# Performance work log

Hardware: AMD Instinct MI355X
Metric: run time of the kernel (lower is better)

## Reference

```python
import jax, jax.numpy as jnp
import numpy as np

# Straight-through sign binarization: forward -> {-1, +1}, backward -> identity
@jax.custom_vjp
def binarize(x):
    return jnp.where(x >= 0, jnp.ones_like(x), -jnp.ones_like(x))

def _bin_fwd(x):
    return binarize(x), None

def _bin_bwd(res, g):
    return (g,)

binarize.defvjp(_bin_fwd, _bin_bwd)

BATCH = 16384
IN_SIZE = 1025   # must be 2**n + 1
HIDDEN = 1025    # must be 2**n + 1

def setup_inputs() -> dict:
    key = jax.random.key(0)
    k0, k1, k2, k3 = jax.random.split(key, 4)
    # weight init scale per reset_parameters: sqrt(1.5/(in+out)) uniform
    s = float(np.sqrt(1.5 / (IN_SIZE + HIDDEN)))
    return {
        "x": jax.random.normal(k0, (BATCH, IN_SIZE), dtype=jnp.float32),
        "W0": jax.random.uniform(k1, (HIDDEN, IN_SIZE), jnp.float32, -s, s),
        "W1": jax.random.uniform(k2, (HIDDEN, HIDDEN), jnp.float32, -s, s),
        "W2": jax.random.uniform(k3, (1, HIDDEN), jnp.float32, -s, s),
    }

def reference(x, W0, W1, W2):
    # x: [B, IN_SIZE]; weights stored [out, in] (nn.Linear convention), no bias
    h = x.reshape(-1, IN_SIZE)
    for W in (W0, W1, W2):
        lin = h @ binarize(W).T          # float GEMM against +/-1 weights
        h = binarize(lin)                # sign activation
    # num_classes == 2 path: to_boolean maps {-1,+1} -> {0,1}, then squeeze
    out = (h + 1.0) * 0.5
    return out.squeeze(-1)               # [B]
```

## Files before the change

### kernel.cpp

```cpp
#include <hip/hip_runtime.h>
#include <cstdint>

typedef unsigned long long u64;
typedef unsigned short ushort_t;
typedef __attribute__((ext_vector_type(8))) short short8;
typedef __attribute__((ext_vector_type(4))) float f32x4;

#define B_TOTAL 16384
#define K_DIM   1025
#define O_DIM   1025
#define NWORDS  17
#define NKT     34
#define NFRAG   72
#define A_BYTES 8192
#define B_BYTES 73728
#define SMEM_BYTES 99328
#define FLAG_CAP 4096
#define L23_ROWS 16

__device__ __forceinline__ ushort_t f2bf_rne(float f) {
  unsigned u = __float_as_uint(f);
  return (ushort_t)((u + 0x7fffu + ((u >> 16) & 1u)) >> 16);
}

__global__ __launch_bounds__(256) void pack_all_kernel(const float* __restrict__ W0,
                                                       const float* __restrict__ W1,
                                                       const float* __restrict__ W2,
                                                       u64* __restrict__ w0b,
                                                       u64* __restrict__ w1b,
                                                       u64* __restrict__ w2b) {
  __shared__ unsigned char by[136];
  const int row = blockIdx.x, t = threadIdx.x;
  const float* src; u64* dst; int o;
  if (row < O_DIM)           { src = W0; dst = w0b; o = row; }
  else if (row < 2 * O_DIM)  { src = W1; dst = w1b; o = row - O_DIM; }
  else                       { src = W2; dst = w2b; o = 0; }
  if (t < 136) {
    const float* wr = src + (size_t)o * K_DIM;
    unsigned m = 0;
#pragma unroll
    for (int j = 0; j < 8; ++j) {
      int k = t * 8 + j;
      bool pos = (k < K_DIM) ? (wr[k] >= 0.0f) : true;
      m |= (unsigned)pos << j;
    }
    by[t] = (unsigned char)m;
  }
  __syncthreads();
  if (t < NWORDS) {
    u64 word = 0;
#pragma unroll
    for (int q = 0; q < 8; ++q) word |= (u64)by[t * 8 + q] << (8 * q);
    dst[(size_t)o * NWORDS + t] = word;
  }
}

__global__ __launch_bounds__(256) void prep_sbf_kernel(const float* __restrict__ w0,
                                                       ushort_t* __restrict__ sbf) {
  const int t = threadIdx.x;
  const int f = blockIdx.x * 4 + (t >> 6);
  const int lane = t & 63;
  const int kt = f / NFRAG, nf = f % NFRAG;
  const int o = nf * 16 + (lane & 15);
  const int kbase = kt * 32 + (lane >> 4) * 8;
  short8 sv;
#pragma unroll
  for (int j = 0; j < 8; ++j) {
    int k = kbase + j;
    short v = 0;
    if (o < O_DIM && k < K_DIM)
      v = (short)((w0[(size_t)o * K_DIM + k] >= 0.0f) ? 0x3F80 : 0xBF80);
    sv[j] = v;
  }
  *(short8*)&sbf[(size_t)f * 512 + lane * 8] = sv;
}

__global__ __launch_bounds__(512, 1) void l1_fused_kernel(
    const ushort_t* __restrict__ sbf, const float* __restrict__ x,
    const u64* __restrict__ w0b, u64* __restrict__ h1b) {
  extern __shared__ char smem[];
  const int p = blockIdx.x;
  const int t = threadIdx.x;
  const int wave = t >> 6, lane = t & 63;
  const int lr = lane & 15, lg = lane >> 4;
  const int b0 = p * 64;
  const int obase = wave * 144;

  const int u = t & 255;
  const int cmf = u >> 6, clane = u & 63;
  const int crow = cmf * 16 + (clane & 15);
  const int ckb0 = (clane >> 4) * 8;
  const bool isLo = (t >= 256);
  const float* xrowC = x + (size_t)(b0 + crow) * K_DIM;
  const int convOff = (isLo ? 4096 : 0) + cmf * 1024 + clane * 16;

  const ushort_t* gB = sbf + (size_t)(wave * 9) * 512 + lane * 8;

  f32x4 acc[4][9];
#pragma unroll
  for (int mf = 0; mf < 4; ++mf)
#pragma unroll
    for (int nfl = 0; nfl < 9; ++nfl)
#pragma unroll
      for (int c = 0; c < 4; ++c) acc[mf][nfl][c] = 0.0f;

  float xv[8];
  float sAcc = 0.0f;
  short8 bX[9];

#define LOADX(KT)                                                              \
  {                                                                            \
    int kb = (KT) * 32 + ckb0;                                                 \
    const float* xr = xrowC + kb;                                              \
    if (kb + 8 <= K_DIM) {                                                     \
      float4 a = *(const float4*)xr;                                           \
      float4 b = *(const float4*)(xr + 4);                                     \
      xv[0]=a.x; xv[1]=a.y; xv[2]=a.z; xv[3]=a.w;                              \
      xv[4]=b.x; xv[5]=b.y; xv[6]=b.z; xv[7]=b.w;                              \
    } else {                                                                   \
      _Pragma("unroll")                                                        \
      for (int j = 0; j < 8; ++j) xv[j] = (kb + j < K_DIM) ? xr[j] : 0.0f;     \
    }                                                                          \
  }

#define CONVERT_WRITE(DBUF)                                                    \
  {                                                                            \
    short8 w8;                                                                 \
    if (!isLo) {                                                               \
      _Pragma("unroll")                                                        \
      for (int j = 0; j < 8; ++j) {                                            \
        float v = xv[j];                                                       \
        sAcc += fabsf(v);                                                      \
        w8[j] = (short)f2bf_rne(v);                                            \
      }                                                                        \
    } else {                                                                   \
      _Pragma("unroll")                                                        \
      for (int j = 0; j < 8; ++j) {                                            \
        float v = xv[j];                                                       \
        ushort_t h = f2bf_rne(v);                                              \
        float hf = __uint_as_float((unsigned)h << 16);                         \
        w8[j] = (short)f2bf_rne(v - hf);                                       \
      }                                                                        \
    }                                                                          \
    *(short8*)((DBUF) + convOff) = w8;                                         \
  }

#define LOADB(KT)                                                              \
  {                                                                            \
    _Pragma("unroll")                                                          \
    for (int i = 0; i < 9; ++i)                                                \
      bX[i] = *(const short8*)&gB[(size_t)(KT) * (B_BYTES / 2) + i * 512];     \
  }

#define MFMA_STEP(AOFF)                                                        \
  {                                                                            \
    const ushort_t* A = (const ushort_t*)(smem + (AOFF));                      \
    short8 ah[4], al[4];                                                       \
    _Pragma("unroll")                                                          \
    for (int mf = 0; mf < 4; ++mf) {                                           \
      ah[mf] = *(const short8*)&A[mf * 512 + lane * 8];                        \
      al[mf] = *(const short8*)&A[(4 + mf) * 512 + lane * 8];                  \
    }                                                                          \
    _Pragma("unroll")                                                          \
    for (int nfl = 0; nfl < 9; ++nfl) {                                        \
      _Pragma("unroll")                                                        \
      for (int mf = 0; mf < 4; ++mf) {                                         \
        acc[mf][nfl] = __builtin_amdgcn_mfma_f32_16x16x32_bf16(ah[mf], bX[nfl], acc[mf][nfl], 0, 0, 0); \
        acc[mf][nfl] = __builtin_amdgcn_mfma_f32_16x16x32_bf16(al[mf], bX[nfl], acc[mf][nfl], 0, 0, 0); \
      }                                                                        \
    }                                                                          \
  }

  LOADX(0); CONVERT_WRITE(smem);
  LOADB(0);
  __syncthreads();

  for (int kt = 0; kt < NKT; kt += 2) {
    {
      LOADX(kt + 1);
      MFMA_STEP(0);
      LOADB(kt + 1);
      CONVERT_WRITE(smem + 8192);
      __syncthreads();
    }
    {
      if (kt + 2 < NKT) LOADX(kt + 2);
      MFMA_STEP(8192);
      if (kt + 2 < NKT) { LOADB(kt + 2); CONVERT_WRITE(smem + 0); }
      __syncthreads();
    }
  }
#undef LOADX
#undef CONVERT_WRITE
#undef LOADB
#undef MFMA_STEP

  unsigned char* bits = (unsigned char*)smem;
  u64*      hs    = (u64*)(smem + 73728);
  unsigned* list  = (unsigned*)(smem + 82432);
  unsigned* lcnt  = (unsigned*)(smem + 98816);
  float*    errbL = (float*)(smem + 98832);
  unsigned* hsw   = (unsigned*)hs;

  sAcc += __shfl_xor(sAcc, 16, 64);
  sAcc += __shfl_xor(sAcc, 32, 64);
  if (t == 0) *lcnt = 0;
  if (!isLo && lg == 0)
    errbL[crow] = sAcc * (1.02f / 65536.0f) + 0.125f;
  __syncthreads();

  float eb[4][4];
#pragma unroll
  for (int mf = 0; mf < 4; ++mf)
#pragma unroll
    for (int rg = 0; rg < 4; ++rg) eb[mf][rg] = errbL[mf * 16 + lg * 4 + rg];

#pragma unroll
  for (int mf = 0; mf < 4; ++mf)
#pragma unroll
    for (int nfl = 0; nfl < 9; ++nfl)
#pragma unroll
      for (int rg = 0; rg < 4; ++rg) {
        int bl = mf * 16 + lg * 4 + rg;
        int o  = obase + nfl * 16 + lr;
        float lin = acc[mf][nfl][rg];
        unsigned abit = (lin >= 0.0f) ? 1u : 0u;
        bits[bl * 1152 + o] = (unsigned char)abit;
        if ((o < O_DIM) && (fabsf(lin) <= eb[mf][rg])) {
          unsigned idx = atomicAdd(lcnt, 1u);
          if (idx < FLAG_CAP)
            list[idx] = ((unsigned)bl << 12) | ((unsigned)o << 1) | abit;
        }
      }
  __syncthreads();

  for (int task = t; task < 64 * NWORDS; task += 512) {
    int row = task / NWORDS, w = task % NWORDS;
    u64 word = 0;
#pragma unroll
    for (int q = 0; q < 8; ++q) {
      u64 v = *(const u64*)&bits[row * 1152 + w * 64 + q * 8];
#pragma unroll
      for (int m = 0; m < 8; ++m)
        word |= ((v >> (8 * m)) & 1ull) << (q * 8 + m);
    }
    int rem = O_DIM - w * 64;
    if (rem < 64) word |= (~0ull << rem);
    hs[row * NWORDS + w] = word;
  }
  __syncthreads();

  {
    unsigned n = *lcnt; if (n > FLAG_CAP) n = FLAG_CAP;
    for (unsigned i = t; i < n; i += 512) {
      unsigned en = list[i];
      int bl = (int)(en >> 12), o = (int)((en >> 1) & 0x7ffu);
      unsigned abit = en & 1u;
      const float* xr = x + (size_t)(b0 + bl) * K_DIM;
      const u64* wr = w0b + (size_t)o * NWORDS;
      float a = 0.0f;
      for (int j = 0; j < 16; ++j) {
        u64 wd = wr[j];
#pragma unroll
        for (int m = 0; m < 64; ++m) {
          float v = xr[j * 64 + m];
          unsigned neg = ((unsigned)(wd >> m) & 1u) ^ 1u;
          a += __uint_as_float(__float_as_uint(v) ^ (neg << 31));
        }
      }
      {
        u64 wd = wr[16];
        float v = xr[1024];
        unsigned neg = ((unsigned)wd & 1u) ^ 1u;
        a += __uint_as_float(__float_as_uint(v) ^ (neg << 31));
      }
      unsigned nb = (a >= 0.0f) ? 1u : 0u;
      if (nb != abit)
        atomicXor(&hsw[bl * 34 + (o >> 5)], 1u << (o & 31));
    }
  }
  __syncthreads();

  for (int task = t; task < 64 * NWORDS; task += 512)
    h1b[(size_t)b0 * NWORDS + task] = hs[task];
}

__global__ __launch_bounds__(256) void l2l3_kernel(const u64* __restrict__ h1b,
                                                   const u64* __restrict__ w1b,
                                                   const u64* __restrict__ w2b,
                                                   float* __restrict__ out) {
  __shared__ u64 hs[L23_ROWS][NWORDS];
  __shared__ u64 h2[L23_ROWS][NWORDS];
  const int bt = blockIdx.x;
  const int t = threadIdx.x;
  for (int i = t; i < L23_ROWS * NWORDS; i += 256)
    hs[i / NWORDS][i % NWORDS] = h1b[(size_t)(bt * L23_ROWS + i / NWORDS) * NWORDS + i % NWORDS];
  __syncthreads();

  const int w = t >> 6, l = t & 63;
  for (int oc = w; oc < NWORDS; oc += 4) {
    int o = oc * 64 + l;
    bool valid = (o < O_DIM);
    int orow = valid ? o : (O_DIM - 1);
    u64 wb[NWORDS];
#pragma unroll
    for (int j = 0; j < NWORDS; ++j) wb[j] = w1b[(size_t)orow * NWORDS + j];
    for (int b = 0; b < L23_ROWS; b += 2) {
      int p0 = 0, p1 = 0;
#pragma unroll
      for (int j = 0; j < NWORDS; ++j) {
        p0 += __popcll(hs[b + 0][j] ^ wb[j]);
        p1 += __popcll(hs[b + 1][j] ^ wb[j]);
      }
      u64 m0 = __ballot(valid ? (K_DIM - 2 * p0 >= 0) : true);
      u64 m1 = __ballot(valid ? (K_DIM - 2 * p1 >= 0) : true);
      if (l == 0) h2[b + 0][oc] = m0;
      if (l == 1) h2[b + 1][oc] = m1;
    }
  }
  __syncthreads();
  if (t < L23_ROWS) {
    int p = 0;
#pragma unroll
    for (int j = 0; j < NWORDS; ++j) p += __popcll(h2[t][j] ^ w2b[j]);
    out[bt * L23_ROWS + t] = ((K_DIM - 2 * p) >= 0) ? 1.0f : 0.0f;
  }
}

extern "C" void kernel_launch(void* const* d_in, const int* in_sizes, int n_in,
                              void* d_out, int out_size, void* d_ws, size_t ws_size,
                              hipStream_t stream) {
  const float* x  = (const float*)d_in[0];
  const float* W0 = (const float*)d_in[1];
  const float* W1 = (const float*)d_in[2];
  const float* W2 = (const float*)d_in[3];
  float* out = (float*)d_out;

  char* ws = (char*)d_ws;
  u64*      w0b  = (u64*)(ws);
  u64*      w1b  = (u64*)(ws + 139776);
  u64*      w2b  = (u64*)(ws + 279552);
  u64*      h1b  = (u64*)(ws + 280064);
  ushort_t* sbf  = (ushort_t*)(ws + 2508288);

  static bool attr_set = false;
  if (!attr_set) {
    hipFuncSetAttribute((const void*)l1_fused_kernel,
                        hipFuncAttributeMaxDynamicSharedMemorySize, SMEM_BYTES);
    attr_set = true;
  }

  pack_all_kernel<<<2 * O_DIM + 1, 256, 0, stream>>>(W0, W1, W2, w0b, w1b, w2b);
  prep_sbf_kernel<<<NKT * NFRAG / 4, 256, 0, stream>>>(W0, sbf);
  l1_fused_kernel<<<B_TOTAL / 64, 512, SMEM_BYTES, stream>>>(sbf, x, w0b, h1b);
  l2l3_kernel<<<B_TOTAL / L23_ROWS, 256, 0, stream>>>(h1b, w1b, w2b, out);
}
```

Baseline: 153.3 us.

## Split layer-1 GEMM output columns across three blocks to raise occupancy

The fused layer-1 kernel now launches a 2D grid where each block computes one third of the output columns (384) for its 64 batch rows, cutting accumulators from 36 to 12 fragments per wave and shared memory from ~97KB to ~36KB. Launch bounds change to allow 4 blocks per CU, so more waves can hide memory latency. The cost is that each x tile is loaded and bf16-split three times (once per column slice), the error-bound reduction is recomputed per block, and the bit-packing, flag list and fix-up are adjusted to per-slice indexing with a smaller flag capacity.

```diff
diff --git a/kernel.cpp b/kernel.cpp
--- a/kernel.cpp
+++ b/kernel.cpp
@@ -14,8 +14,9 @@
 #define NFRAG   72
 #define A_BYTES 8192
 #define B_BYTES 73728
-#define SMEM_BYTES 99328
-#define FLAG_CAP 4096
+#define NS      3
+#define SMEM_BYTES 36352
+#define FLAG_CAP 2048
 #define L23_ROWS 16
 
 __device__ __forceinline__ ushort_t f2bf_rne(float f) {
@@ -75,16 +76,16 @@
   *(short8*)&sbf[(size_t)f * 512 + lane * 8] = sv;
 }
 
-__global__ __launch_bounds__(512, 1) void l1_fused_kernel(
+__global__ __launch_bounds__(512, 4) void l1_fused_kernel(
     const ushort_t* __restrict__ sbf, const float* __restrict__ x,
     const u64* __restrict__ w0b, u64* __restrict__ h1b) {
   extern __shared__ char smem[];
-  const int p = blockIdx.x;
+  const int p = blockIdx.x, ns = blockIdx.y;
   const int t = threadIdx.x;
   const int wave = t >> 6, lane = t & 63;
   const int lr = lane & 15, lg = lane >> 4;
   const int b0 = p * 64;
-  const int obase = wave * 144;
+  const int obase_l = wave * 48;
 
   const int u = t & 255;
   const int cmf = u >> 6, clane = u & 63;
@@ -94,19 +95,19 @@
   const float* xrowC = x + (size_t)(b0 + crow) * K_DIM;
   const int convOff = (isLo ? 4096 : 0) + cmf * 1024 + clane * 16;
 
-  const ushort_t* gB = sbf + (size_t)(wave * 9) * 512 + lane * 8;
-
-  f32x4 acc[4][9];
+  const ushort_t* gB = sbf + (size_t)(ns * 24 + wave * 3) * 512 + lane * 8;
+
+  f32x4 acc[4][3];
 #pragma unroll
   for (int mf = 0; mf < 4; ++mf)
 #pragma unroll
-    for (int nfl = 0; nfl < 9; ++nfl)
+    for (int nfl = 0; nfl < 3; ++nfl)
 #pragma unroll
       for (int c = 0; c < 4; ++c) acc[mf][nfl][c] = 0.0f;
 
   float xv[8];
   float sAcc = 0.0f;
-  short8 bX[9];
+  short8 bX[3];
 
 #define LOADX(KT)                                                              \
   {                                                                            \
@@ -148,25 +149,29 @@
 #define LOADB(KT)                                                              \
   {                                                                            \
     _Pragma("unroll")                                                          \
-    for (int i = 0; i < 9; ++i)                                                \
+    for (int i = 0; i < 3; ++i)                                                \
       bX[i] = *(const short8*)&gB[(size_t)(KT) * (B_BYTES / 2) + i * 512];     \
   }
 
 #define MFMA_STEP(AOFF)                                                        \
   {                                                                            \
     const ushort_t* A = (const ushort_t*)(smem + (AOFF));                      \
-    short8 ah[4], al[4];                                                       \
     _Pragma("unroll")                                                          \
-    for (int mf = 0; mf < 4; ++mf) {                                           \
-      ah[mf] = *(const short8*)&A[mf * 512 + lane * 8];                        \
-      al[mf] = *(const short8*)&A[(4 + mf) * 512 + lane * 8];                  \
-    }                                                                          \
-    _Pragma("unroll")                                                          \
-    for (int nfl = 0; nfl < 9; ++nfl) {                                        \
-      _Pragma("unroll")                                                        \
-      for (int mf = 0; mf < 4; ++mf) {                                         \
-        acc[mf][nfl] = __builtin_amdgcn_mfma_f32_16x16x32_bf16(ah[mf], bX[nfl], acc[mf][nfl], 0, 0, 0); \
-        acc[mf][nfl] = __builtin_amdgcn_mfma_f32_16x16x32_bf16(al[mf], bX[nfl], acc[mf][nfl], 0, 0, 0); \
+    for (int h = 0; h < 2; ++h) {                                              \
+      short8 ah2[2], al2[2];                                                   \
+      _Pragma("unroll")                                                        \
+      for (int m2 = 0; m2 < 2; ++m2) {                                         \
+        ah2[m2] = *(const short8*)&A[(h * 2 + m2) * 512 + lane * 8];           \
+        al2[m2] = *(const short8*)&A[(4 + h * 2 + m2) * 512 + lane * 8];       \
+      }                                                                        \
+      _Pragma("unroll")                                                        \
+      for (int nfl = 0; nfl < 3; ++nfl) {                                      \
+        _Pragma("unroll")                                                      \
+        for (int m2 = 0; m2 < 2; ++m2) {                                       \
+          int mf = h * 2 + m2;                                                 \
+          acc[mf][nfl] = __builtin_amdgcn_mfma_f32_16x16x32_bf16(ah2[m2], bX[nfl], acc[mf][nfl], 0, 0, 0); \
+          acc[mf][nfl] = __builtin_amdgcn_mfma_f32_16x16x32_bf16(al2[m2], bX[nfl], acc[mf][nfl], 0, 0, 0); \
+        }                                                                      \
       }                                                                        \
     }                                                                          \
   }
@@ -196,10 +201,10 @@
 #undef MFMA_STEP
 
   unsigned char* bits = (unsigned char*)smem;
-  u64*      hs    = (u64*)(smem + 73728);
-  unsigned* list  = (unsigned*)(smem + 82432);
-  unsigned* lcnt  = (unsigned*)(smem + 98816);
-  float*    errbL = (float*)(smem + 98832);
+  u64*      hs    = (u64*)(smem + 24576);
+  unsigned* list  = (unsigned*)(smem + 27648);
+  unsigned* lcnt  = (unsigned*)(smem + 35840);
+  float*    errbL = (float*)(smem + 35844);
   unsigned* hsw   = (unsigned*)hs;
 
   sAcc += __shfl_xor(sAcc, 16, 64);
@@ -218,35 +223,38 @@
 #pragma unroll
   for (int mf = 0; mf < 4; ++mf)
 #pragma unroll
-    for (int nfl = 0; nfl < 9; ++nfl)
+    for (int nfl = 0; nfl < 3; ++nfl)
 #pragma unroll
       for (int rg = 0; rg < 4; ++rg) {
         int bl = mf * 16 + lg * 4 + rg;
-        int o  = obase + nfl * 16 + lr;
+        int ol = obase_l + nfl * 16 + lr;
+        int og = ns * 384 + ol;
         float lin = acc[mf][nfl][rg];
         unsigned abit = (lin >= 0.0f) ? 1u : 0u;
-        bits[bl * 1152 + o] = (unsigned char)abit;
-        if ((o < O_DIM) && (fabsf(lin) <= eb[mf][rg])) {
+        bits[bl * 384 + ol] = (unsigned char)abit;
+        if ((og < O_DIM) && (fabsf(lin) <= eb[mf][rg])) {
           unsigned idx = atomicAdd(lcnt, 1u);
           if (idx < FLAG_CAP)
-            list[idx] = ((unsigned)bl << 12) | ((unsigned)o << 1) | abit;
+            list[idx] = ((unsigned)bl << 12) | ((unsigned)ol << 1) | abit;
         }
       }
   __syncthreads();
 
-  for (int task = t; task < 64 * NWORDS; task += 512) {
-    int row = task / NWORDS, w = task % NWORDS;
+  if (t < 64 * 6) {
+    int row = t / 6, w = t % 6;
+    int widx = ns * 6 + w;
     u64 word = 0;
 #pragma unroll
     for (int q = 0; q < 8; ++q) {
-      u64 v = *(const u64*)&bits[row * 1152 + w * 64 + q * 8];
+      u64 v = *(const u64*)&bits[row * 384 + w * 64 + q * 8];
 #pragma unroll
       for (int m = 0; m < 8; ++m)
         word |= ((v >> (8 * m)) & 1ull) << (q * 8 + m);
     }
-    int rem = O_DIM - w * 64;
-    if (rem < 64) word |= (~0ull << rem);
-    hs[row * NWORDS + w] = word;
+    int rem = O_DIM - widx * 64;
+    if (rem <= 0) word = ~0ull;
+    else if (rem < 64) word |= (~0ull << rem);
+    hs[row * 6 + w] = word;
   }
   __syncthreads();
 
@@ -254,10 +262,11 @@
     unsigned n = *lcnt; if (n > FLAG_CAP) n = FLAG_CAP;
     for (unsigned i = t; i < n; i += 512) {
       unsigned en = list[i];
-      int bl = (int)(en >> 12), o = (int)((en >> 1) & 0x7ffu);
+      int bl = (int)(en >> 12), ol = (int)((en >> 1) & 0x7ffu);
+      int og = ns * 384 + ol;
       unsigned abit = en & 1u;
       const float* xr = x + (size_t)(b0 + bl) * K_DIM;
-      const u64* wr = w0b + (size_t)o * NWORDS;
+      const u64* wr = w0b + (size_t)og * NWORDS;
       float a = 0.0f;
       for (int j = 0; j < 16; ++j) {
         u64 wd = wr[j];
@@ -276,13 +285,17 @@
       }
       unsigned nb = (a >= 0.0f) ? 1u : 0u;
       if (nb != abit)
-        atomicXor(&hsw[bl * 34 + (o >> 5)], 1u << (o & 31));
-    }
-  }
-  __syncthreads();
-
-  for (int task = t; task < 64 * NWORDS; task += 512)
-    h1b[(size_t)b0 * NWORDS + task] = hs[task];
+        atomicXor(&hsw[bl * 12 + (ol >> 5)], 1u << (ol & 31));
+    }
+  }
+  __syncthreads();
+
+  if (t < 64 * 6) {
+    int row = t / 6, w = t % 6;
+    int widx = ns * 6 + w;
+    if (widx < NWORDS)
+      h1b[(size_t)(b0 + row) * NWORDS + widx] = hs[t];
+  }
 }
 
 __global__ __launch_bounds__(256) void l2l3_kernel(const u64* __restrict__ h1b,
@@ -352,6 +365,6 @@
 
   pack_all_kernel<<<2 * O_DIM + 1, 256, 0, stream>>>(W0, W1, W2, w0b, w1b, w2b);
   prep_sbf_kernel<<<NKT * NFRAG / 4, 256, 0, stream>>>(W0, sbf);
-  l1_fused_kernel<<<B_TOTAL / 64, 512, SMEM_BYTES, stream>>>(sbf, x, w0b, h1b);
+  l1_fused_kernel<<<dim3(B_TOTAL / 64, NS), 512, SMEM_BYTES, stream>>>(sbf, x, w0b, h1b);
   l2l3_kernel<<<B_TOTAL / L23_ROWS, 256, 0, stream>>>(h1b, w1b, w2b, out);
 }
```

Result: slower. 217.9 us (+42.1%).

## Halve layer-1 row tile to 32 and stream B fragments to raise occupancy

Applied to the files above, without the earlier changes.

Shrinks the fused layer-1 GEMM tile from 64 to 32 batch rows per block, halving accumulators and LDS (about 49KB instead of 99KB). The launch bound moves from 1 to 4 blocks per CU and the grid doubles. B fragments are no longer held in a full 9-register prefetch; they are loaded from global memory through a 4-deep rotating register window inside the MFMA step. The intent is more resident waves to hide latency, at the cost of each B fragment being read from global/L2 twice as often across the grid.

```diff
diff --git a/kernel.cpp b/kernel.cpp
--- a/kernel.cpp
+++ b/kernel.cpp
@@ -4,6 +4,7 @@
 typedef unsigned long long u64;
 typedef unsigned short ushort_t;
 typedef __attribute__((ext_vector_type(8))) short short8;
+typedef __attribute__((ext_vector_type(4))) short short4v;
 typedef __attribute__((ext_vector_type(4))) float f32x4;
 
 #define B_TOTAL 16384
@@ -12,10 +13,10 @@
 #define NWORDS  17
 #define NKT     34
 #define NFRAG   72
-#define A_BYTES 8192
 #define B_BYTES 73728
-#define SMEM_BYTES 99328
-#define FLAG_CAP 4096
+#define BM      32
+#define SMEM_BYTES 49920
+#define FLAG_CAP 2048
 #define L23_ROWS 16
 
 __device__ __forceinline__ ushort_t f2bf_rne(float f) {
@@ -75,7 +76,7 @@
   *(short8*)&sbf[(size_t)f * 512 + lane * 8] = sv;
 }
 
-__global__ __launch_bounds__(512, 1) void l1_fused_kernel(
+__global__ __launch_bounds__(512, 4) void l1_fused_kernel(
     const ushort_t* __restrict__ sbf, const float* __restrict__ x,
     const u64* __restrict__ w0b, u64* __restrict__ h1b) {
   extern __shared__ char smem[];
@@ -83,140 +84,134 @@
   const int t = threadIdx.x;
   const int wave = t >> 6, lane = t & 63;
   const int lr = lane & 15, lg = lane >> 4;
-  const int b0 = p * 64;
+  const int b0 = p * BM;
   const int obase = wave * 144;
 
   const int u = t & 255;
-  const int cmf = u >> 6, clane = u & 63;
+  const int slot = u >> 1, half = u & 1;
+  const int cmf = slot >> 6, clane = slot & 63;
   const int crow = cmf * 16 + (clane & 15);
-  const int ckb0 = (clane >> 4) * 8;
+  const int ckb0 = (clane >> 4) * 8 + half * 4;
   const bool isLo = (t >= 256);
   const float* xrowC = x + (size_t)(b0 + crow) * K_DIM;
-  const int convOff = (isLo ? 4096 : 0) + cmf * 1024 + clane * 16;
+  const int convOff = (isLo ? 2048 : 0) + cmf * 1024 + clane * 16 + half * 8;
 
   const ushort_t* gB = sbf + (size_t)(wave * 9) * 512 + lane * 8;
 
-  f32x4 acc[4][9];
-#pragma unroll
-  for (int mf = 0; mf < 4; ++mf)
+  f32x4 acc[2][9];
+#pragma unroll
+  for (int mf = 0; mf < 2; ++mf)
 #pragma unroll
     for (int nfl = 0; nfl < 9; ++nfl)
 #pragma unroll
       for (int c = 0; c < 4; ++c) acc[mf][nfl][c] = 0.0f;
 
-  float xv[8];
+  float xv[4];
   float sAcc = 0.0f;
-  short8 bX[9];
 
 #define LOADX(KT)                                                              \
   {                                                                            \
     int kb = (KT) * 32 + ckb0;                                                 \
     const float* xr = xrowC + kb;                                              \
-    if (kb + 8 <= K_DIM) {                                                     \
+    if (kb + 4 <= K_DIM) {                                                     \
       float4 a = *(const float4*)xr;                                           \
-      float4 b = *(const float4*)(xr + 4);                                     \
-      xv[0]=a.x; xv[1]=a.y; xv[2]=a.z; xv[3]=a.w;                              \
-      xv[4]=b.x; xv[5]=b.y; xv[6]=b.z; xv[7]=b.w;                              \
+      xv[0] = a.x; xv[1] = a.y; xv[2] = a.z; xv[3] = a.w;                      \
     } else {                                                                   \
       _Pragma("unroll")                                                        \
-      for (int j = 0; j < 8; ++j) xv[j] = (kb + j < K_DIM) ? xr[j] : 0.0f;     \
+      for (int j = 0; j < 4; ++j) xv[j] = (kb + j < K_DIM) ? xr[j] : 0.0f;     \
     }                                                                          \
   }
 
 #define CONVERT_WRITE(DBUF)                                                    \
   {                                                                            \
-    short8 w8;                                                                 \
+    short4v w4;                                                                \
     if (!isLo) {                                                               \
       _Pragma("unroll")                                                        \
-      for (int j = 0; j < 8; ++j) {                                            \
+      for (int j = 0; j < 4; ++j) {                                            \
         float v = xv[j];                                                       \
         sAcc += fabsf(v);                                                      \
-        w8[j] = (short)f2bf_rne(v);                                            \
+        w4[j] = (short)f2bf_rne(v);                                            \
       }                                                                        \
     } else {                                                                   \
       _Pragma("unroll")                                                        \
-      for (int j = 0; j < 8; ++j) {                                            \
+      for (int j = 0; j < 4; ++j) {                                            \
         float v = xv[j];                                                       \
         ushort_t h = f2bf_rne(v);                                              \
         float hf = __uint_as_float((unsigned)h << 16);                         \
-        w8[j] = (short)f2bf_rne(v - hf);                                       \
+        w4[j] = (short)f2bf_rne(v - hf);                                       \
       }                                                                        \
     }                                                                          \
-    *(short8*)((DBUF) + convOff) = w8;                                         \
-  }
-
-#define LOADB(KT)                                                              \
-  {                                                                            \
-    _Pragma("unroll")                                                          \
-    for (int i = 0; i < 9; ++i)                                                \
-      bX[i] = *(const short8*)&gB[(size_t)(KT) * (B_BYTES / 2) + i * 512];     \
-  }
-
-#define MFMA_STEP(AOFF)                                                        \
+    *(short4v*)((DBUF) + convOff) = w4;                                        \
+  }
+
+#define MFMA_STEP(AOFF, KT)                                                    \
   {                                                                            \
     const ushort_t* A = (const ushort_t*)(smem + (AOFF));                      \
-    short8 ah[4], al[4];                                                       \
-    _Pragma("unroll")                                                          \
-    for (int mf = 0; mf < 4; ++mf) {                                           \
-      ah[mf] = *(const short8*)&A[mf * 512 + lane * 8];                        \
-      al[mf] = *(const short8*)&A[(4 + mf) * 512 + lane * 8];                  \
-    }                                                                          \
+    const ushort_t* gBkt = gB + (size_t)(KT) * (B_BYTES / 2);                  \
+    short8 ah0 = *(const short8*)&A[lane * 8];                                 \
+    short8 ah1 = *(const short8*)&A[512 + lane * 8];                           \
+    short8 al0 = *(const short8*)&A[1024 + lane * 8];                          \
+    short8 al1 = *(const short8*)&A[1536 + lane * 8];                          \
+    short8 bR[4];                                                              \
+    bR[0] = *(const short8*)&gBkt[0];                                          \
+    bR[1] = *(const short8*)&gBkt[512];                                        \
+    bR[2] = *(const short8*)&gBkt[1024];                                       \
     _Pragma("unroll")                                                          \
     for (int nfl = 0; nfl < 9; ++nfl) {                                        \
-      _Pragma("unroll")                                                        \
-      for (int mf = 0; mf < 4; ++mf) {                                         \
-        acc[mf][nfl] = __builtin_amdgcn_mfma_f32_16x16x32_bf16(ah[mf], bX[nfl], acc[mf][nfl], 0, 0, 0); \
-        acc[mf][nfl] = __builtin_amdgcn_mfma_f32_16x16x32_bf16(al[mf], bX[nfl], acc[mf][nfl], 0, 0, 0); \
-      }                                                                        \
+      if (nfl < 6) bR[(nfl + 3) & 3] = *(const short8*)&gBkt[(nfl + 3) * 512]; \
+      short8 bv = bR[nfl & 3];                                                 \
+      acc[0][nfl] = __builtin_amdgcn_mfma_f32_16x16x32_bf16(ah0, bv, acc[0][nfl], 0, 0, 0); \
+      acc[0][nfl] = __builtin_amdgcn_mfma_f32_16x16x32_bf16(al0, bv, acc[0][nfl], 0, 0, 0); \
+      acc[1][nfl] = __builtin_amdgcn_mfma_f32_16x16x32_bf16(ah1, bv, acc[1][nfl], 0, 0, 0); \
+      acc[1][nfl] = __builtin_amdgcn_mfma_f32_16x16x32_bf16(al1, bv, acc[1][nfl], 0, 0, 0); \
     }                                                                          \
   }
 
   LOADX(0); CONVERT_WRITE(smem);
-  LOADB(0);
   __syncthreads();
 
   for (int kt = 0; kt < NKT; kt += 2) {
-    {
-      LOADX(kt + 1);
-      MFMA_STEP(0);
-      LOADB(kt + 1);
-      CONVERT_WRITE(smem + 8192);
-      __syncthreads();
-    }
-    {
-      if (kt + 2 < NKT) LOADX(kt + 2);
-      MFMA_STEP(8192);
-      if (kt + 2 < NKT) { LOADB(kt + 2); CONVERT_WRITE(smem + 0); }
-      __syncthreads();
-    }
+    LOADX(kt + 1);
+    MFMA_STEP(0, kt);
+    CONVERT_WRITE(smem + 4096);
+    __syncthreads();
+    if (kt + 2 < NKT) LOADX(kt + 2);
+    MFMA_STEP(4096, kt + 1);
+    if (kt + 2 < NKT) CONVERT_WRITE(smem);
+    __syncthreads();
   }
 #undef LOADX
 #undef CONVERT_WRITE
-#undef LOADB
 #undef MFMA_STEP
 
   unsigned char* bits = (unsigned char*)smem;
-  u64*      hs    = (u64*)(smem + 73728);
-  unsigned* list  = (unsigned*)(smem + 82432);
-  unsigned* lcnt  = (unsigned*)(smem + 98816);
-  float*    errbL = (float*)(smem + 98832);
+  u64*      hs    = (u64*)(smem + 36864);
+  unsigned* list  = (unsigned*)(smem + 41216);
+  unsigned* lcnt  = (unsigned*)(smem + 49408);
+  float*    errbP = (float*)(smem + 49412);
+  float*    errbL = (float*)(smem + 49668);
   unsigned* hsw   = (unsigned*)hs;
 
-  sAcc += __shfl_xor(sAcc, 16, 64);
+  sAcc += __shfl_xor(sAcc, 1, 64);
   sAcc += __shfl_xor(sAcc, 32, 64);
   if (t == 0) *lcnt = 0;
-  if (!isLo && lg == 0)
-    errbL[crow] = sAcc * (1.02f / 65536.0f) + 0.125f;
-  __syncthreads();
-
-  float eb[4][4];
-#pragma unroll
-  for (int mf = 0; mf < 4; ++mf)
+  if (!isLo && (lane & 1) == 0 && lane < 32)
+    errbP[wave * 16 + (lane >> 1)] = sAcc;
+  __syncthreads();
+  if (t < BM) {
+    int cm = t >> 4, R = t & 15;
+    errbL[t] = (errbP[cm * 32 + R] + errbP[cm * 32 + 16 + R]) * (1.02f / 65536.0f) + 0.125f;
+  }
+  __syncthreads();
+
+  float eb[2][4];
+#pragma unroll
+  for (int mf = 0; mf < 2; ++mf)
 #pragma unroll
     for (int rg = 0; rg < 4; ++rg) eb[mf][rg] = errbL[mf * 16 + lg * 4 + rg];
 
 #pragma unroll
-  for (int mf = 0; mf < 4; ++mf)
+  for (int mf = 0; mf < 2; ++mf)
 #pragma unroll
     for (int nfl = 0; nfl < 9; ++nfl)
 #pragma unroll
@@ -234,7 +229,7 @@
       }
   __syncthreads();
 
-  for (int task = t; task < 64 * NWORDS; task += 512) {
+  for (int task = t; task < BM * NWORDS; task += 512) {
     int row = task / NWORDS, w = task % NWORDS;
     u64 word = 0;
 #pragma unroll
@@ -246,7 +241,7 @@
     }
     int rem = O_DIM - w * 64;
     if (rem < 64) word |= (~0ull << rem);
-    hs[row * NWORDS + w] = word;
+    hs[task] = word;
   }
   __syncthreads();
 
@@ -281,7 +276,7 @@
   }
   __syncthreads();
 
-  for (int task = t; task < 64 * NWORDS; task += 512)
+  for (int task = t; task < BM * NWORDS; task += 512)
     h1b[(size_t)b0 * NWORDS + task] = hs[task];
 }
 
@@ -352,6 +347,6 @@
 
   pack_all_kernel<<<2 * O_DIM + 1, 256, 0, stream>>>(W0, W1, W2, w0b, w1b, w2b);
   prep_sbf_kernel<<<NKT * NFRAG / 4, 256, 0, stream>>>(W0, sbf);
-  l1_fused_kernel<<<B_TOTAL / 64, 512, SMEM_BYTES, stream>>>(sbf, x, w0b, h1b);
+  l1_fused_kernel<<<B_TOTAL / BM, 512, SMEM_BYTES, stream>>>(sbf, x, w0b, h1b);
   l2l3_kernel<<<B_TOTAL / L23_ROWS, 256, 0, stream>>>(h1b, w1b, w2b, out);
 }
```

Result: slower. 173.6 us (+13.2%).
